# Kernel optimization log

Hardware: AMD Instinct MI355X
Metric: run time of the kernel (lower is better)

## Reference

```python
import jax, jax.numpy as jnp
import numpy as np

N = 4096          # number of cells
M = 8             # number of morphogen channels
FOUR_PI = 4.0 * np.pi
EPS = 1e-8


def setup_inputs() -> dict:
    key = jax.random.key(0)
    k1, k2, k3, k4 = jax.random.split(key, 4)
    position = jax.random.uniform(k1, (N, 3), dtype=jnp.float32) * 100.0   # cells in a 100^3 box
    radius = 0.5 + jax.random.uniform(k2, (N,), dtype=jnp.float32) * 0.5   # cell radii in [0.5, 1.0]
    secretion = jax.random.uniform(k3, (N, M), dtype=jnp.float32)          # per-cell source strengths
    active = jax.random.randint(k4, (N,), 0, 2) > 0                        # bool mask on source cells
    diffusion_coefs = jnp.asarray([0.5, 1.0, 2.0, 4.0, 0.25, 1.5, 3.0, 0.75], dtype=jnp.float32)
    degradation_rates = jnp.asarray([0.01, 0.02, 0.005, 0.04, 0.01, 0.03, 0.008, 0.02], dtype=jnp.float32)
    return {
        "position": position,
        "radius": radius,
        "secretion": secretion,
        "diffusion_coefs": diffusion_coefs,
        "degradation_rates": degradation_rates,
        "active": active,
    }


def reference(position, radius, secretion, diffusion_coefs, degradation_rates, active):
    # Pairwise distances [N, N]; clamp below by source-cell radius to avoid the
    # 1/r singularity at the self term (field evaluated at the cell surface).
    diff = position[:, None, :] - position[None, :, :]            # [N, N, 3]
    dist = jnp.sqrt(jnp.sum(diff * diff, axis=-1) + EPS)          # [N, N]
    dist = jnp.maximum(dist, radius[None, :])                     # clamp by source radius

    # Steady-state 3D diffusion-degradation Green's function per morphogen m:
    #   G_m(r) = exp(-r / lambda_m) / (4 pi D_m r),  lambda_m = sqrt(D_m / k_m)
    lam = jnp.sqrt(diffusion_coefs / degradation_rates)           # [M]
    d = dist[:, :, None]                                          # [N, N, 1]
    kernel = jnp.exp(-d / lam) / (FOUR_PI * diffusion_coefs * d)  # [N, N, M]

    # Only active cells secrete.
    src = secretion * active[:, None].astype(secretion.dtype)     # [N, M]
    concentrations = jnp.einsum("ijm,jm->im", kernel, src)        # [N, M]
    return concentrations
```

## Files before the change

kernel.cpp:

```cpp
#include <hip/hip_runtime.h>
#include <math.h>

#define NN 4096
#define MM 8
#define BLOCK 256
#define IPT 2
#define IBLK (BLOCK * IPT)
#define CC 128
#define JT 32
#define FOUR_PI_F 12.566370614359172f
#define EPS_F 1e-8f
#define LOG2E_F 1.4426950408889634f


template <int VAR>
__device__ __forceinline__ void run_tile(
    int nact, const float4* __restrict__ sj, const float4* __restrict__ ss,
    const float* __restrict__ px, const float* __restrict__ py,
    const float* __restrict__ pz, const float* __restrict__ na,
    float acc[IPT][MM])
{
#pragma unroll 2
    for (int jj = 0; jj < nact; ++jj) {
        const float4 pj = sj[jj];
        const float4 s0 = ss[jj * 2 + 0];
        const float4 s1 = ss[jj * 2 + 1];
#pragma unroll
        for (int r = 0; r < IPT; ++r) {
            float dx = px[r] - pj.x;
            float dy = py[r] - pj.y;
            float dz = pz[r] - pj.z;
            float d2 = fmaf(dx, dx, fmaf(dy, dy, fmaf(dz, dz, EPS_F)));
            float d2c = fmaxf(d2, pj.w);
            float rs = __builtin_amdgcn_rsqf(d2c);
            float dcl = d2c * rs;

            float f[MM];
            if constexpr (VAR == 2) {
                float eA = __builtin_amdgcn_exp2f(dcl * na[0]);
                float e2 = __builtin_amdgcn_exp2f(dcl * na[2]);
                float e3 = e2 * e2;
                float e4 = e3 * e3;
                float e6 = __builtin_amdgcn_exp2f(dcl * na[6]);
                float e7 = __builtin_amdgcn_exp2f(dcl * na[7]);
                float fA = eA * rs;
                f[0] = fA; f[1] = fA; f[5] = fA;
                f[2] = e2 * rs; f[3] = e3 * rs; f[4] = e4 * rs;
                f[6] = e6 * rs; f[7] = e7 * rs;
            } else if constexpr (VAR == 1) {
                float fA = __builtin_amdgcn_exp2f(dcl * na[0]) * rs;
                f[0] = fA; f[1] = fA; f[5] = fA;
                f[2] = __builtin_amdgcn_exp2f(dcl * na[2]) * rs;
                f[3] = __builtin_amdgcn_exp2f(dcl * na[3]) * rs;
                f[4] = __builtin_amdgcn_exp2f(dcl * na[4]) * rs;
                f[6] = __builtin_amdgcn_exp2f(dcl * na[6]) * rs;
                f[7] = __builtin_amdgcn_exp2f(dcl * na[7]) * rs;
            } else {
#pragma unroll
                for (int m = 0; m < MM; ++m)
                    f[m] = __builtin_amdgcn_exp2f(dcl * na[m]) * rs;
            }

            const float s[MM] = {s0.x, s0.y, s0.z, s0.w,
                                 s1.x, s1.y, s1.z, s1.w};
#pragma unroll
            for (int m = 0; m < MM; ++m)
                acc[r][m] = fmaf(f[m], s[m], acc[r][m]);
        }
    }
}

__global__ __launch_bounds__(BLOCK) void diff_partial(
    const float* __restrict__ pos, const float* __restrict__ radius,
    const float* __restrict__ secretion, const float* __restrict__ Dc,
    const float* __restrict__ Kd, const int* __restrict__ active,
    float* __restrict__ partial,
    int ntiles)
{
    __shared__ float4 sj[JT];
    __shared__ float4 ss[JT * 2];
    __shared__ int s_nact;

    const int tid = threadIdx.x;
    const int i0 = blockIdx.x * IBLK + tid;
    const int i1 = i0 + BLOCK;
    const int j0base = blockIdx.y * (JT * ntiles);

    float na[MM], invD[MM];
    float acc[IPT][MM];
#pragma unroll
    for (int m = 0; m < MM; ++m) {
        float lam = sqrtf(Dc[m] / Kd[m]);
        na[m] = -LOG2E_F / lam;
        invD[m] = 1.0f / (FOUR_PI_F * Dc[m]);
        acc[0][m] = 0.0f; acc[1][m] = 0.0f;
    }
    const bool dup015 = (na[0] == na[1]) && (na[0] == na[5]);
    const bool chain =
        dup015 &&
        (fabsf(na[3] - 2.0f * na[2]) <= 4e-6f * fabsf(na[3])) &&
        (fabsf(na[4] - 2.0f * na[3]) <= 4e-6f * fabsf(na[4]));

    const float px[IPT] = {pos[i0 * 3 + 0], pos[i1 * 3 + 0]};
    const float py[IPT] = {pos[i0 * 3 + 1], pos[i1 * 3 + 1]};
    const float pz[IPT] = {pos[i0 * 3 + 2], pos[i1 * 3 + 2]};

    for (int t = 0; t < ntiles; ++t) {
        const int j0 = j0base + t * JT;
        __syncthreads();

        if (tid < JT) {
            const int j = j0 + tid;
            const bool act = (active[j] != 0);
            const unsigned long long mask = __ballot(act);
            if (tid == 0) s_nact = __popcll(mask);
            if (act) {
                const int k = __popcll(mask & ((1ull << tid) - 1ull));
                const float r = radius[j];
                sj[k] = make_float4(pos[j * 3 + 0], pos[j * 3 + 1],
                                    pos[j * 3 + 2], r * r);
                const float4 s0 =
                    reinterpret_cast<const float4*>(secretion)[j * 2 + 0];
                const float4 s1 =
                    reinterpret_cast<const float4*>(secretion)[j * 2 + 1];
                ss[k * 2 + 0] = make_float4(s0.x * invD[0], s0.y * invD[1],
                                            s0.z * invD[2], s0.w * invD[3]);
                ss[k * 2 + 1] = make_float4(s1.x * invD[4], s1.y * invD[5],
                                            s1.z * invD[6], s1.w * invD[7]);
            }
        }
        __syncthreads();

        const int nact = s_nact;
        if (chain)       run_tile<2>(nact, sj, ss, px, py, pz, na, acc);
        else if (dup015) run_tile<1>(nact, sj, ss, px, py, pz, na, acc);
        else             run_tile<0>(nact, sj, ss, px, py, pz, na, acc);
    }

    float* base = partial + (size_t)blockIdx.y * NN * MM;
    float4* d0 = reinterpret_cast<float4*>(base + (size_t)i0 * MM);
    float4* d1 = reinterpret_cast<float4*>(base + (size_t)i1 * MM);
    d0[0] = make_float4(acc[0][0], acc[0][1], acc[0][2], acc[0][3]);
    d0[1] = make_float4(acc[0][4], acc[0][5], acc[0][6], acc[0][7]);
    d1[0] = make_float4(acc[1][0], acc[1][1], acc[1][2], acc[1][3]);
    d1[1] = make_float4(acc[1][4], acc[1][5], acc[1][6], acc[1][7]);
}

__global__ __launch_bounds__(BLOCK) void diff_reduce(
    const float4* __restrict__ partial, float4* __restrict__ out, int C)
{
    __shared__ float4 red[4][64];
    const int tx = threadIdx.x & 63;
    const int ty = threadIdx.x >> 6;
    const int o = blockIdx.x * 64 + tx;

    float4 s = make_float4(0.f, 0.f, 0.f, 0.f);
    for (int c = ty; c < C; c += 4) {
        const float4 p = partial[(size_t)c * (NN * MM / 4) + o];
        s.x += p.x; s.y += p.y; s.z += p.z; s.w += p.w;
    }
    red[ty][tx] = s;
    __syncthreads();
    if (ty == 0) {
        const float4 a = red[1][tx], b = red[2][tx], c4 = red[3][tx];
        s.x += a.x + b.x + c4.x;
        s.y += a.y + b.y + c4.y;
        s.z += a.z + b.z + c4.z;
        s.w += a.w + b.w + c4.w;
        out[o] = s;
    }
}

extern "C" void kernel_launch(void* const* d_in, const int* in_sizes, int n_in,
                              void* d_out, int out_size, void* d_ws, size_t ws_size,
                              hipStream_t stream) {
    const float* pos       = (const float*)d_in[0];
    const float* radius    = (const float*)d_in[1];
    const float* secretion = (const float*)d_in[2];
    const float* Dc        = (const float*)d_in[3];
    const float* Kd        = (const float*)d_in[4];
    const int*   active    = (const int*)d_in[5];
    float* out = (float*)d_out;

    const size_t slice = (size_t)NN * MM * sizeof(float);

    int C = CC;
    while (C > 4 && (size_t)C * slice > ws_size) C >>= 1;
    const int ntiles = NN / (C * JT);

    float* partial = (float*)d_ws;
    dim3 grid(NN / IBLK, C);
    diff_partial<<<grid, BLOCK, 0, stream>>>(pos, radius, secretion, Dc, Kd,
                                             active, partial, ntiles);
    diff_reduce<<<NN * MM / 4 / 64, BLOCK, 0, stream>>>(
        (const float4*)partial, (float4*)out, C);
}
```

Measured before the change: 90.77 us.

## Use one target cell per thread, larger source tiles, fewer partial slices

Each thread now handles a single target cell instead of two. Source tiles grow from 32 to 64 and the number of j-chunks drops from 128 to 64, so the block count stays the same. This halves the partial-sum buffer that has to be written and then reduced. The reduction kernel becomes a 16x16 shared-memory tree over more, smaller blocks. The cost is less reuse of each shared-memory source load across rows and less per-thread ILP.

```diff
diff --git a/kernel.cpp b/kernel.cpp
--- a/kernel.cpp
+++ b/kernel.cpp
@@ -4,10 +4,8 @@
 #define NN 4096
 #define MM 8
 #define BLOCK 256
-#define IPT 2
-#define IBLK (BLOCK * IPT)
-#define CC 128
-#define JT 32
+#define CC 64
+#define JT 64
 #define FOUR_PI_F 12.566370614359172f
 #define EPS_F 1e-8f
 #define LOG2E_F 1.4426950408889634f
@@ -16,57 +14,52 @@
 template <int VAR>
 __device__ __forceinline__ void run_tile(
     int nact, const float4* __restrict__ sj, const float4* __restrict__ ss,
-    const float* __restrict__ px, const float* __restrict__ py,
-    const float* __restrict__ pz, const float* __restrict__ na,
-    float acc[IPT][MM])
+    float px, float py, float pz, const float* __restrict__ na,
+    float* __restrict__ acc)
 {
 #pragma unroll 2
     for (int jj = 0; jj < nact; ++jj) {
         const float4 pj = sj[jj];
         const float4 s0 = ss[jj * 2 + 0];
         const float4 s1 = ss[jj * 2 + 1];
-#pragma unroll
-        for (int r = 0; r < IPT; ++r) {
-            float dx = px[r] - pj.x;
-            float dy = py[r] - pj.y;
-            float dz = pz[r] - pj.z;
-            float d2 = fmaf(dx, dx, fmaf(dy, dy, fmaf(dz, dz, EPS_F)));
-            float d2c = fmaxf(d2, pj.w);
-            float rs = __builtin_amdgcn_rsqf(d2c);
-            float dcl = d2c * rs;
+        float dx = px - pj.x;
+        float dy = py - pj.y;
+        float dz = pz - pj.z;
+        float d2 = fmaf(dx, dx, fmaf(dy, dy, fmaf(dz, dz, EPS_F)));
+        float d2c = fmaxf(d2, pj.w);
+        float rs = __builtin_amdgcn_rsqf(d2c);
+        float dcl = d2c * rs;
 
-            float f[MM];
-            if constexpr (VAR == 2) {
-                float eA = __builtin_amdgcn_exp2f(dcl * na[0]);
-                float e2 = __builtin_amdgcn_exp2f(dcl * na[2]);
-                float e3 = e2 * e2;
-                float e4 = e3 * e3;
-                float e6 = __builtin_amdgcn_exp2f(dcl * na[6]);
-                float e7 = __builtin_amdgcn_exp2f(dcl * na[7]);
-                float fA = eA * rs;
-                f[0] = fA; f[1] = fA; f[5] = fA;
-                f[2] = e2 * rs; f[3] = e3 * rs; f[4] = e4 * rs;
-                f[6] = e6 * rs; f[7] = e7 * rs;
-            } else if constexpr (VAR == 1) {
-                float fA = __builtin_amdgcn_exp2f(dcl * na[0]) * rs;
-                f[0] = fA; f[1] = fA; f[5] = fA;
-                f[2] = __builtin_amdgcn_exp2f(dcl * na[2]) * rs;
-                f[3] = __builtin_amdgcn_exp2f(dcl * na[3]) * rs;
-                f[4] = __builtin_amdgcn_exp2f(dcl * na[4]) * rs;
-                f[6] = __builtin_amdgcn_exp2f(dcl * na[6]) * rs;
-                f[7] = __builtin_amdgcn_exp2f(dcl * na[7]) * rs;
-            } else {
-#pragma unroll
-                for (int m = 0; m < MM; ++m)
-                    f[m] = __builtin_amdgcn_exp2f(dcl * na[m]) * rs;
-            }
-
-            const float s[MM] = {s0.x, s0.y, s0.z, s0.w,
-                                 s1.x, s1.y, s1.z, s1.w};
+        float f[MM];
+        if constexpr (VAR == 2) {
+            float eA = __builtin_amdgcn_exp2f(dcl * na[0]);
+            float e2 = __builtin_amdgcn_exp2f(dcl * na[2]);
+            float e3 = e2 * e2;
+            float e4 = e3 * e3;
+            float e6 = __builtin_amdgcn_exp2f(dcl * na[6]);
+            float e7 = __builtin_amdgcn_exp2f(dcl * na[7]);
+            float fA = eA * rs;
+            f[0] = fA; f[1] = fA; f[5] = fA;
+            f[2] = e2 * rs; f[3] = e3 * rs; f[4] = e4 * rs;
+            f[6] = e6 * rs; f[7] = e7 * rs;
+        } else if constexpr (VAR == 1) {
+            float fA = __builtin_amdgcn_exp2f(dcl * na[0]) * rs;
+            f[0] = fA; f[1] = fA; f[5] = fA;
+            f[2] = __builtin_amdgcn_exp2f(dcl * na[2]) * rs;
+            f[3] = __builtin_amdgcn_exp2f(dcl * na[3]) * rs;
+            f[4] = __builtin_amdgcn_exp2f(dcl * na[4]) * rs;
+            f[6] = __builtin_amdgcn_exp2f(dcl * na[6]) * rs;
+            f[7] = __builtin_amdgcn_exp2f(dcl * na[7]) * rs;
+        } else {
 #pragma unroll
             for (int m = 0; m < MM; ++m)
-                acc[r][m] = fmaf(f[m], s[m], acc[r][m]);
+                f[m] = __builtin_amdgcn_exp2f(dcl * na[m]) * rs;
         }
+
+        const float s[MM] = {s0.x, s0.y, s0.z, s0.w, s1.x, s1.y, s1.z, s1.w};
+#pragma unroll
+        for (int m = 0; m < MM; ++m)
+            acc[m] = fmaf(f[m], s[m], acc[m]);
     }
 }
 
@@ -82,18 +75,16 @@
     __shared__ int s_nact;
 
     const int tid = threadIdx.x;
-    const int i0 = blockIdx.x * IBLK + tid;
-    const int i1 = i0 + BLOCK;
+    const int i = blockIdx.x * BLOCK + tid;
     const int j0base = blockIdx.y * (JT * ntiles);
 
-    float na[MM], invD[MM];
-    float acc[IPT][MM];
+    float na[MM], invD[MM], acc[MM];
 #pragma unroll
     for (int m = 0; m < MM; ++m) {
         float lam = sqrtf(Dc[m] / Kd[m]);
         na[m] = -LOG2E_F / lam;
         invD[m] = 1.0f / (FOUR_PI_F * Dc[m]);
-        acc[0][m] = 0.0f; acc[1][m] = 0.0f;
+        acc[m] = 0.0f;
     }
     const bool dup015 = (na[0] == na[1]) && (na[0] == na[5]);
     const bool chain =
@@ -101,9 +92,9 @@
         (fabsf(na[3] - 2.0f * na[2]) <= 4e-6f * fabsf(na[3])) &&
         (fabsf(na[4] - 2.0f * na[3]) <= 4e-6f * fabsf(na[4]));
 
-    const float px[IPT] = {pos[i0 * 3 + 0], pos[i1 * 3 + 0]};
-    const float py[IPT] = {pos[i0 * 3 + 1], pos[i1 * 3 + 1]};
-    const float pz[IPT] = {pos[i0 * 3 + 2], pos[i1 * 3 + 2]};
+    const float px = pos[i * 3 + 0];
+    const float py = pos[i * 3 + 1];
+    const float pz = pos[i * 3 + 2];
 
     for (int t = 0; t < ntiles; ++t) {
         const int j0 = j0base + t * JT;
@@ -137,38 +128,37 @@
         else             run_tile<0>(nact, sj, ss, px, py, pz, na, acc);
     }
 
-    float* base = partial + (size_t)blockIdx.y * NN * MM;
-    float4* d0 = reinterpret_cast<float4*>(base + (size_t)i0 * MM);
-    float4* d1 = reinterpret_cast<float4*>(base + (size_t)i1 * MM);
-    d0[0] = make_float4(acc[0][0], acc[0][1], acc[0][2], acc[0][3]);
-    d0[1] = make_float4(acc[0][4], acc[0][5], acc[0][6], acc[0][7]);
-    d1[0] = make_float4(acc[1][0], acc[1][1], acc[1][2], acc[1][3]);
-    d1[1] = make_float4(acc[1][4], acc[1][5], acc[1][6], acc[1][7]);
+    float4* dst = reinterpret_cast<float4*>(
+        partial + (size_t)blockIdx.y * NN * MM + (size_t)i * MM);
+    dst[0] = make_float4(acc[0], acc[1], acc[2], acc[3]);
+    dst[1] = make_float4(acc[4], acc[5], acc[6], acc[7]);
 }
 
 __global__ __launch_bounds__(BLOCK) void diff_reduce(
     const float4* __restrict__ partial, float4* __restrict__ out, int C)
 {
-    __shared__ float4 red[4][64];
-    const int tx = threadIdx.x & 63;
-    const int ty = threadIdx.x >> 6;
-    const int o = blockIdx.x * 64 + tx;
+    __shared__ float4 red[16][16];
+    const int tx = threadIdx.x & 15;
+    const int ty = threadIdx.x >> 4;
+    const int o = blockIdx.x * 16 + tx;
 
     float4 s = make_float4(0.f, 0.f, 0.f, 0.f);
-    for (int c = ty; c < C; c += 4) {
+    for (int c = ty; c < C; c += 16) {
         const float4 p = partial[(size_t)c * (NN * MM / 4) + o];
         s.x += p.x; s.y += p.y; s.z += p.z; s.w += p.w;
     }
     red[ty][tx] = s;
     __syncthreads();
-    if (ty == 0) {
-        const float4 a = red[1][tx], b = red[2][tx], c4 = red[3][tx];
-        s.x += a.x + b.x + c4.x;
-        s.y += a.y + b.y + c4.y;
-        s.z += a.z + b.z + c4.z;
-        s.w += a.w + b.w + c4.w;
-        out[o] = s;
+#pragma unroll
+    for (int h = 8; h >= 1; h >>= 1) {
+        if (ty < h) {
+            float4 a = red[ty + h][tx];
+            red[ty][tx].x += a.x; red[ty][tx].y += a.y;
+            red[ty][tx].z += a.z; red[ty][tx].w += a.w;
+        }
+        __syncthreads();
     }
+    if (ty == 0) out[o] = red[0][tx];
 }
 
 extern "C" void kernel_launch(void* const* d_in, const int* in_sizes, int n_in,
@@ -189,9 +179,9 @@
     const int ntiles = NN / (C * JT);
 
     float* partial = (float*)d_ws;
-    dim3 grid(NN / IBLK, C);
+    dim3 grid(NN / BLOCK, C);
     diff_partial<<<grid, BLOCK, 0, stream>>>(pos, radius, secretion, Dc, Kd,
                                              active, partial, ntiles);
-    diff_reduce<<<NN * MM / 4 / 64, BLOCK, 0, stream>>>(
+    diff_reduce<<<(NN * MM / 4) / 16, BLOCK, 0, stream>>>(
         (const float4*)partial, (float4*)out, C);
 }
```

After: 80.72 us. 11.1% less time.
